# Kernel tuning notes

Measured on AMD Instinct MI355X. Metric: run time of the kernel, lower is better.

The kernel has to match this reference:

```python
import jax, jax.numpy as jnp
import numpy as np

# ---- static config (mirrors init_kwargs) ----
H, N, HKV = 32, 64, 8
HN = H * N            # model dim 2048
KV_DIM = HKV * N      # 512
B, T = 2, 1024
EPS = 1e-6
ROPE_THETA = 1.0e6
SPLITS_WAVGK = (96, 96, 64, 256, 64)   # xw, xa, xv, xg, xk lora ranks
SPLITS_RKV = (HN, KV_DIM, KV_DIM)


def rms_norm(x, w, eps=EPS):
    xf = x.astype(jnp.float32)
    var = jnp.mean(xf * xf, axis=-1, keepdims=True)
    return (w * (xf * jax.lax.rsqrt(var + eps))).astype(x.dtype)


def rotate_half(x):
    x1, x2 = jnp.split(x, 2, axis=-1)
    return jnp.concatenate((-x2, x1), axis=-1)


def apply_rope(q, k, cos, sin):
    # q:[B,T,H,N], k:[B,T,HKV,N], cos/sin:[B,T,N] -> unsqueeze head dim (unsqueeze_dim=2)
    cos = cos[:, :, None, :]
    sin = sin[:, :, None, :]
    return q * cos + rotate_half(q) * sin, k * cos + rotate_half(k) * sin


def rwkv7_recurrence(r, gk, k, v, a, b, S0):
    # fused_recurrent_rwkv7 (head_first=False). All inputs [B,T,H,N] fp32, S0 [B,H,N_key,N_val].
    # S_t = diag(exp(gk_t)) S_{t-1} + b_t (a_t^T S_{t-1}) + k_t v_t^T ;  o_t = r_t^T S_t
    def step(S, inp):
        r_t, w_t, k_t, v_t, a_t, b_t = inp
        sa = jnp.einsum('bhk,bhkv->bhv', a_t, S)
        S = (jnp.exp(w_t)[..., None] * S
             + k_t[..., None] * v_t[..., None, :]
             + b_t[..., None] * sa[..., None, :])
        o = jnp.einsum('bhk,bhkv->bhv', r_t, S)
        return S, o
    xs = tuple(jnp.swapaxes(t, 0, 1) for t in (r, gk, k, v, a, b))  # [T,B,H,N]
    S, o = jax.lax.scan(step, S0, xs)
    return jnp.swapaxes(o, 0, 1), S


def setup_inputs() -> dict:
    key = jax.random.key(0)
    ks = jax.random.split(key, 24)
    f32 = jnp.float32
    rn = lambda k, shape, s=1.0: jax.random.normal(k, shape, dtype=f32) * s

    x_in = rn(ks[0], (B, T, HN))
    v_first = rn(ks[1], (B, T, HKV, N))
    k_first = rn(ks[2], (B, T, HKV, N))
    state = jnp.zeros((B, H, N, N), f32)

    # real rope cache (faithful to get_batch_rope_cache output) at positions 0..T-1
    inv_freq = 1.0 / (ROPE_THETA ** (np.arange(0, N, 2, dtype=np.float32) / N))
    freqs = np.outer(np.arange(T, dtype=np.float32), inv_freq)  # [T, N/2]
    emb = np.concatenate([freqs, freqs], axis=-1)               # [T, N]
    calc_cos = jnp.broadcast_to(jnp.asarray(np.cos(emb), dtype=np.float32), (B, T, N))
    calc_sin = jnp.broadcast_to(jnp.asarray(np.sin(emb), dtype=np.float32), (B, T, N))

    wavgk1 = rn(ks[3], (HN, sum(SPLITS_WAVGK)), 0.02)
    w0 = rn(ks[4], (HN,), 0.5)
    w2 = rn(ks[5], (SPLITS_WAVGK[0], HN), 0.02)
    a0 = rn(ks[6], (HN,), 0.1)
    a2 = rn(ks[7], (SPLITS_WAVGK[1], HN), 0.02)
    v0 = rn(ks[8], (KV_DIM,), 0.1)
    v2 = rn(ks[9], (SPLITS_WAVGK[2], KV_DIM), 0.02)
    g2 = rn(ks[10], (SPLITS_WAVGK[3], HN), 0.02)
    k0 = rn(ks[11], (KV_DIM,), 0.1)
    k2 = rn(ks[12], (SPLITS_WAVGK[4], KV_DIM), 0.02)
    r_k = rn(ks[13], (H, N), 0.1)
    RKV = rn(ks[14], (HN, HN + 2 * KV_DIM), 0.02)   # fpx weight, dequantized form
    O = rn(ks[15], (HN, HN), 0.02)
    R_bias = rn(ks[16], (HN,), 0.02)
    K_bias = rn(ks[17], (KV_DIM,), 0.02)
    V_bias = rn(ks[18], (KV_DIM,), 0.02)
    ln_r = jnp.ones((N,), f32)
    ln_k = jnp.ones((N,), f32)
    ln1 = jnp.ones((HN,), f32)
    ln2 = jnp.ones((HN,), f32)

    return dict(x_in=x_in, v_first=v_first, k_first=k_first, state=state,
                calc_cos=calc_cos, calc_sin=calc_sin, wavgk1=wavgk1,
                w0=w0, w2=w2, a0=a0, a2=a2, v0=v0, v2=v2, g2=g2, k0=k0, k2=k2,
                r_k=r_k, RKV=RKV, O=O, R_bias=R_bias, K_bias=K_bias, V_bias=V_bias,
                ln_r=ln_r, ln_k=ln_k, ln1=ln1, ln2=ln2)


def reference(x_in, v_first, k_first, state, calc_cos, calc_sin, wavgk1,
              w0, w2, a0, a2, v0, v2, g2, k0, k2, r_k, RKV, O,
              R_bias, K_bias, V_bias, ln_r, ln_k, ln1, ln2):
    Bx, Tx, C = x_in.shape
    kv_repeat = HN // KV_DIM  # GQA repeat factor (4)

    x = rms_norm(x_in, ln1)
    xw, xa, xv, xg, xk = jnp.split(x @ wavgk1, np.cumsum(SPLITS_WAVGK)[:-1].tolist(), axis=-1)

    rkv = x @ RKV  # fpx_matmul -> dense matmul on dequantized weight
    r, k, v = jnp.split(rkv, np.cumsum(SPLITS_RKV)[:-1].tolist(), axis=-1)
    r = (r + R_bias).reshape(Bx, Tx, H, N)
    k = (k + K_bias).reshape(Bx, Tx, HKV, N)
    v = (v + V_bias).reshape(Bx, Tx, HKV, N)

    r = rms_norm(r, ln_r)
    k = rms_norm(k, ln_k)
    r, k = apply_rope(r, k, calc_cos, calc_sin)

    # layer_id = 1 (> 0): mix with first-layer value/key
    v = v + (v_first - v) * jax.nn.sigmoid(xv @ v2 + v0).reshape(Bx, Tx, HKV, N)
    k = k + (k_first - k) * jax.nn.sigmoid(xk @ k2 + k0).reshape(Bx, Tx, HKV, N)

    # repeat_kv: [B,T,HKV,N] -> [B,T,H,N] -> [B,T,HN]
    k = jnp.repeat(k, kv_repeat, axis=2).reshape(Bx, Tx, HN)
    v = jnp.repeat(v, kv_repeat, axis=2).reshape(Bx, Tx, HN)

    a = jax.nn.sigmoid(xa @ a2 + a0)  # in-context learning rate gate [B,T,HN]
    k4 = k.reshape(Bx, Tx, H, N)
    kk = (k4 / jnp.maximum(jnp.linalg.norm(k4, axis=-1, keepdims=True), 1e-12)).reshape(Bx, Tx, HN)

    w_log = -jax.nn.softplus(-(jnp.tanh(xw) @ w2 + w0)) - 0.5  # log-decay, <= -0.5
    k = k * (1.0 - w_log + a)
    aa = -kk
    bb = kk * a
    gk = -jnp.exp(w_log.astype(jnp.float32))  # passed to fused_recurrent_rwkv7 as log decay

    shp = (Bx, Tx, H, N)
    o, state_out = rwkv7_recurrence(
        r.reshape(shp).astype(jnp.float32), gk.reshape(shp),
        k.reshape(shp).astype(jnp.float32), v.reshape(shp).astype(jnp.float32),
        aa.reshape(shp).astype(jnp.float32), bb.reshape(shp).astype(jnp.float32),
        state.astype(jnp.float32))

    xx = o.reshape(Bx, Tx, HN) * (float(N) ** -0.5)
    bonus = ((r * k.reshape(shp) * r_k).sum(axis=-1, keepdims=True) * v.reshape(shp)).reshape(Bx, Tx, HN)
    xx = xx.astype(x_in.dtype) + bonus

    out = (xx * (jax.nn.sigmoid(xg) @ g2)) @ O  # fpx output projection
    x_new = x_in + out
    return rms_norm(x_new, ln2)
```

## Files before the change

### kernel.cpp

```cpp
#include <hip/hip_runtime.h>

typedef unsigned short u16;
typedef unsigned int u32;

using f32x4 = __attribute__((ext_vector_type(4))) float;
using bf16x8 = __attribute__((ext_vector_type(8))) __bf16;

#define HN 2048
#define KVD 512
#define TOKENS 2048
#define N1 3712
#define K2W 576
#define N2 7168

#define OFF_Y1   0ull
#define OFF_OO   0ull
#define OFF_XG   16777216ull
#define OFF_Y2   30408704ull
#define OFF_OUTR 30408704ull
#define OFF_BT1  89128960ull
#define OFF_XB   104333312ull
#define OFF_W2T  89128960ull
#define OFF_X2   97386496ull
#define OFF_OT   89128960ull
#define OFF_RR   112721920ull
#define OFF_DEC  129499136ull
#define OFF_KR   146276352ull
#define OFF_VV   163053568ull
#define OFF_AA   179830784ull
#define OFF_BB   196608000ull
#define OFF_PAB  213385216ull
#define OFF_PKR  230162432ull
#define WS_NEED  246939648ull

__device__ __forceinline__ u16 f2bf(float f) {
    u32 u = __float_as_uint(f);
    u32 r = u + 0x7fffu + ((u >> 16) & 1u);
    return (u16)(r >> 16);
}
__device__ __forceinline__ float sigm(float x) { return 1.f / (1.f + expf(-x)); }
__device__ __forceinline__ float wsum(float v) {
#pragma unroll
    for (int m = 32; m > 0; m >>= 1) v += __shfl_xor(v, m, 64);
    return v;
}
__device__ __forceinline__ float rowsum16(float v) {
    float t;
    t = __uint_as_float(__builtin_amdgcn_update_dpp(0, __float_as_uint(v), 0x121, 0xf, 0xf, true));
    v += t;
    t = __uint_as_float(__builtin_amdgcn_update_dpp(0, __float_as_uint(v), 0x122, 0xf, 0xf, true));
    v += t;
    t = __uint_as_float(__builtin_amdgcn_update_dpp(0, __float_as_uint(v), 0x124, 0xf, 0xf, true));
    v += t;
    t = __uint_as_float(__builtin_amdgcn_update_dpp(0, __float_as_uint(v), 0x128, 0xf, 0xf, true));
    v += t;
    return v;
}

typedef __attribute__((address_space(1))) const void glob_t;
typedef __attribute__((address_space(3))) void lds_t;
__device__ __forceinline__ void gload_lds16(const void* g, void* l) {
    __builtin_amdgcn_global_load_lds((glob_t*)g, (lds_t*)l, 16, 0, 0);
}

template<int OFF>
__device__ __forceinline__ float4 ds_read128(u32 a) {
    float4 r;
    asm volatile("ds_read_b128 %0, %1 offset:%2" : "=v"(r) : "v"(a), "i"(OFF));
    return r;
}
template<int OFF>
__device__ __forceinline__ uint4 ds_read128u(u32 a) {
    uint4 r;
    asm volatile("ds_read_b128 %0, %1 offset:%2" : "=v"(r) : "v"(a), "i"(OFF));
    return r;
}
template<int OFF>
__device__ __forceinline__ float ds_read32(u32 a) {
    float r;
    asm volatile("ds_read_b32 %0, %1 offset:%2" : "=v"(r) : "v"(a), "i"(OFF));
    return r;
}

__global__ __launch_bounds__(256) void k_prep_bt1(const float* __restrict__ wavgk1,
                                                  const float* __restrict__ RKV,
                                                  u16* __restrict__ BT1) {
    __shared__ float tile[64][65];
    const int bn = blockIdx.x >> 5;
    const int bk = blockIdx.x & 31;
    const int n0 = bn << 6, k0 = bk << 6;
    const int c = threadIdx.x & 63, q = threadIdx.x >> 6;
#pragma unroll
    for (int i = 0; i < 16; ++i) {
        const int r = (q << 4) + i;
        float v = 0.f;
        if (bn < 9)       v = wavgk1[(size_t)(k0 + r) * 576 + n0 + c];
        else if (bn < 57) v = RKV[(size_t)(k0 + r) * 3072 + (n0 + c - 576)];
        tile[r][c] = v;
    }
    __syncthreads();
#pragma unroll
    for (int i = 0; i < 16; ++i) {
        const int rw = (q << 4) + i;
        BT1[(size_t)(n0 + rw) * 2048 + k0 + c] = f2bf(tile[c][rw]);
    }
}

__global__ __launch_bounds__(256) void k_prep_w2t(const float* __restrict__ w2, const float* __restrict__ a2,
                                                  const float* __restrict__ g2, const float* __restrict__ v2,
                                                  const float* __restrict__ k2, u16* __restrict__ W2T) {
    int idx = blockIdx.x * 256 + threadIdx.x;
    int n = idx / 576, c = idx - n * 576;
    float v = 0.f;
    if (n < 2048)      { if (c < 96)              v = w2[(size_t)c * 2048 + n]; }
    else if (n < 4096) { if (c >= 96 && c < 192)  v = a2[(size_t)(c - 96) * 2048 + (n - 2048)]; }
    else if (n < 6144) { if (c >= 192 && c < 448) v = g2[(size_t)(c - 192) * 2048 + (n - 4096)]; }
    else if (n < 6656) { if (c >= 448 && c < 512) v = v2[(size_t)(c - 448) * 512 + (n - 6144)]; }
    else               { if (c >= 512)            v = k2[(size_t)(c - 512) * 512 + (n - 6656)]; }
    W2T[idx] = f2bf(v);
}

__global__ __launch_bounds__(256) void k_prep_ot(const float* __restrict__ O, u16* __restrict__ OT) {
    __shared__ float tile[64][65];
    const int bn = blockIdx.x >> 5, bk = blockIdx.x & 31;
    const int n0 = bn << 6, k0 = bk << 6;
    const int c = threadIdx.x & 63, q = threadIdx.x >> 6;
#pragma unroll
    for (int i = 0; i < 16; ++i) {
        const int r = (q << 4) + i;
        tile[r][c] = O[(size_t)(k0 + r) * 2048 + n0 + c];
    }
    __syncthreads();
#pragma unroll
    for (int i = 0; i < 16; ++i) {
        const int rw = (q << 4) + i;
        OT[(size_t)(n0 + rw) * 2048 + k0 + c] = f2bf(tile[c][rw]);
    }
}

__global__ __launch_bounds__(256) void k_rms1(const float* __restrict__ X,
                                              const float* __restrict__ ln1,
                                              u16* __restrict__ XB) {
    const int t = blockIdx.x, tid = threadIdx.x;
    const float* row = X + ((size_t)t << 11);
    float4 v0 = *(const float4*)(row + tid * 8);
    float4 v1 = *(const float4*)(row + tid * 8 + 4);
    float ss = v0.x*v0.x + v0.y*v0.y + v0.z*v0.z + v0.w*v0.w
             + v1.x*v1.x + v1.y*v1.y + v1.z*v1.z + v1.w*v1.w;
    ss = wsum(ss);
    __shared__ float red[4];
    if ((tid & 63) == 0) red[tid >> 6] = ss;
    __syncthreads();
    float scale = rsqrtf((red[0] + red[1] + red[2] + red[3]) * (1.f / 2048.f) + 1e-6f);
    float4 w0_ = *(const float4*)(ln1 + tid * 8);
    float4 w1_ = *(const float4*)(ln1 + tid * 8 + 4);
    u16* o = XB + ((size_t)t << 11) + tid * 8;
    o[0] = f2bf(v0.x * scale * w0_.x); o[1] = f2bf(v0.y * scale * w0_.y);
    o[2] = f2bf(v0.z * scale * w0_.z); o[3] = f2bf(v0.w * scale * w0_.w);
    o[4] = f2bf(v1.x * scale * w1_.x); o[5] = f2bf(v1.y * scale * w1_.y);
    o[6] = f2bf(v1.z * scale * w1_.z); o[7] = f2bf(v1.w * scale * w1_.w);
}

__global__ __launch_bounds__(256) void k_gemm(const u16* __restrict__ A,
                                              const u16* __restrict__ Bt,
                                              float* __restrict__ C,
                                              int M, int N, int K) {
    __shared__ __align__(16) u16 tA[4096];
    __shared__ __align__(16) u16 tB[4096];
    const int tid = threadIdx.x;
    const int w = tid >> 6, l = tid & 63;
    const int bm = blockIdx.x << 7, bn = blockIdx.y << 7;
    const int wm = (w >> 1) << 6, wn = (w & 1) << 6;
    const int lrow = l >> 2;
    const int lk = (((l & 3) ^ ((l >> 3) & 3)) << 3);
    f32x4 acc[4][4] = {};
    const size_t rA0 = (size_t)(bm + (w << 4) + lrow) * K;
    const size_t rA1 = (size_t)(bm + ((w + 4) << 4) + lrow) * K;
    const size_t rB0 = (size_t)(bn + (w << 4) + lrow) * K;
    const size_t rB1 = (size_t)(bn + ((w + 4) << 4) + lrow) * K;
    const int frow = l & 15;
    const int koff = (((l >> 4) ^ ((l >> 1) & 3)) << 3);
    for (int kt = 0; kt < K; kt += 32) {
        gload_lds16(A + rA0 + kt + lk, &tA[w << 9]);
        gload_lds16(A + rA1 + kt + lk, &tA[2048 + (w << 9)]);
        gload_lds16(Bt + rB0 + kt + lk, &tB[w << 9]);
        gload_lds16(Bt + rB1 + kt + lk, &tB[2048 + (w << 9)]);
        __syncthreads();
        bf16x8 av[4], bv[4];
#pragma unroll
        for (int i = 0; i < 4; ++i) {
            av[i] = *(const bf16x8*)&tA[((wm + (i << 4) + frow) << 5) + koff];
            bv[i] = *(const bf16x8*)&tB[((wn + (i << 4) + frow) << 5) + koff];
        }
#pragma unroll
        for (int i = 0; i < 4; ++i)
#pragma unroll
            for (int j = 0; j < 4; ++j)
                acc[i][j] = __builtin_amdgcn_mfma_f32_16x16x32_bf16(av[i], bv[j], acc[i][j], 0, 0, 0);
        __syncthreads();
    }
    const int crow = bm + wm + ((l >> 4) << 2);
    const int ccol = bn + wn + (l & 15);
#pragma unroll
    for (int i = 0; i < 4; ++i)
#pragma unroll
        for (int j = 0; j < 4; ++j)
#pragma unroll
            for (int jj = 0; jj < 4; ++jj)
                C[(size_t)(crow + (i << 4) + jj) * N + ccol + (j << 4)] = acc[i][j][jj];
}

__global__ __launch_bounds__(256) void k_gemm2(const u16* __restrict__ A,
                                               const u16* __restrict__ Bt,
                                               float* __restrict__ C) {
    __shared__ __align__(16) u16 tA[4096];
    __shared__ __align__(16) u16 tB[4096];
    const int tid = threadIdx.x;
    const int w = tid >> 6, l = tid & 63;
    const int by = blockIdx.y;
    int c0, K;
    if (by < 16)      { c0 = 0;   K = 96; }
    else if (by < 32) { c0 = 96;  K = 96; }
    else if (by < 48) { c0 = 192; K = 256; }
    else if (by < 52) { c0 = 448; K = 64; }
    else              { c0 = 512; K = 64; }
    const int n0 = by << 7;
    const int bm = blockIdx.x << 7;
    const int wm = (w >> 1) << 6, wn = (w & 1) << 6;
    const int lrow = l >> 2;
    const int lk = (((l & 3) ^ ((l >> 3) & 3)) << 3);
    f32x4 acc[4][4] = {};
    const size_t rA0 = (size_t)(bm + (w << 4) + lrow) * 576 + c0;
    const size_t rA1 = (size_t)(bm + ((w + 4) << 4) + lrow) * 576 + c0;
    const size_t rB0 = (size_t)(n0 + (w << 4) + lrow) * 576 + c0;
    const size_t rB1 = (size_t)(n0 + ((w + 4) << 4) + lrow) * 576 + c0;
    const int frow = l & 15;
    const int koff = (((l >> 4) ^ ((l >> 1) & 3)) << 3);
    for (int kt = 0; kt < K; kt += 32) {
        gload_lds16(A + rA0 + kt + lk, &tA[w << 9]);
        gload_lds16(A + rA1 + kt + lk, &tA[2048 + (w << 9)]);
        gload_lds16(Bt + rB0 + kt + lk, &tB[w << 9]);
        gload_lds16(Bt + rB1 + kt + lk, &tB[2048 + (w << 9)]);
        __syncthreads();
        bf16x8 av[4], bv[4];
#pragma unroll
        for (int i = 0; i < 4; ++i) {
            av[i] = *(const bf16x8*)&tA[((wm + (i << 4) + frow) << 5) + koff];
            bv[i] = *(const bf16x8*)&tB[((wn + (i << 4) + frow) << 5) + koff];
        }
#pragma unroll
        for (int i = 0; i < 4; ++i)
#pragma unroll
            for (int j = 0; j < 4; ++j)
                acc[i][j] = __builtin_amdgcn_mfma_f32_16x16x32_bf16(av[i], bv[j], acc[i][j], 0, 0, 0);
        __syncthreads();
    }
    const int crow = bm + wm + ((l >> 4) << 2);
    const int ccol = n0 + wn + (l & 15);
#pragma unroll
    for (int i = 0; i < 4; ++i)
#pragma unroll
        for (int j = 0; j < 4; ++j)
#pragma unroll
            for (int jj = 0; jj < 4; ++jj)
                C[(size_t)(crow + (i << 4) + jj) * N2 + ccol + (j << 4)] = acc[i][j][jj];
}

__global__ __launch_bounds__(256) void k_prep_x2(const float* __restrict__ Y1, u16* __restrict__ X2) {
    int idx = blockIdx.x * 256 + threadIdx.x;
    int t = idx / 576, c = idx - t * 576;
    const float* y1 = Y1 + (size_t)t * N1;
    float v;
    if (c < 96)       v = tanhf(y1[c]);
    else if (c < 192) v = y1[c];
    else if (c < 448) v = sigm(y1[c + 64]);
    else if (c < 512) v = y1[c - 256];
    else              v = y1[c];
    X2[idx] = f2bf(v);
}

__global__ __launch_bounds__(256) void k_prep_rec(
    const float* __restrict__ Y1, const float* __restrict__ Y2,
    const float* __restrict__ v_first, const float* __restrict__ k_first,
    const float* __restrict__ cosb, const float* __restrict__ sinb,
    const float* __restrict__ w0, const float* __restrict__ a0,
    const float* __restrict__ v0b, const float* __restrict__ k0b,
    const float* __restrict__ R_bias, const float* __restrict__ K_bias,
    const float* __restrict__ V_bias, const float* __restrict__ ln_r,
    const float* __restrict__ ln_k,
    float* __restrict__ RR, float* __restrict__ DEC, float* __restrict__ KR,
    float* __restrict__ VV, u32* __restrict__ PAB, u32* __restrict__ PKR) {
    const int t = blockIdx.x, tid = threadIdx.x;
    const int ww = tid >> 6, lane = tid & 63;
    const float* y1 = Y1 + (size_t)t * N1;
    const float* y2 = Y2 + (size_t)t * N2;
    const float cs = cosb[t * 64 + lane];
    const float sn = sinb[t * 64 + lane];
    const float sign = lane < 32 ? -1.f : 1.f;
    const size_t tb = (size_t)t << 11;
    __shared__ float kkv[512], vkv[512];
    float rsave[8];
#pragma unroll
    for (int i = 0; i < 8; ++i) {
        int h = ww * 8 + i, c = h * 64 + lane;
        float rr = y1[576 + c] + R_bias[c];
        float ssq = wsum(rr * rr);
        float rn = ln_r[lane] * rr * rsqrtf(ssq * (1.f / 64.f) + 1e-6f);
        float rot = sign * __shfl(rn, lane ^ 32, 64);
        rsave[i] = rn * cs + rot * sn;
        RR[tb + c] = rsave[i];
    }
#pragma unroll
    for (int i = 0; i < 2; ++i) {
        int j = ww * 2 + i, c = j * 64 + lane;
        float kr = y1[2624 + c] + K_bias[c];
        float ssq = wsum(kr * kr);
        float kn = ln_k[lane] * kr * rsqrtf(ssq * (1.f / 64.f) + 1e-6f);
        float rot = sign * __shfl(kn, lane ^ 32, 64);
        float krope = kn * cs + rot * sn;
        float ksig = sigm(y2[6656 + c] + k0b[c]);
        kkv[c] = krope + (k_first[(size_t)t * 512 + c] - krope) * ksig;
        float vr = y1[3136 + c] + V_bias[c];
        float vsig = sigm(y2[6144 + c] + v0b[c]);
        vkv[c] = vr + (v_first[(size_t)t * 512 + c] - vr) * vsig;
    }
    __syncthreads();
#pragma unroll
    for (int i = 0; i < 8; ++i) {
        int h = ww * 8 + i, c = h * 64 + lane;
        int ckv = (h >> 2) * 64 + lane;
        float kb = kkv[ckv], vb = vkv[ckv];
        float a_ = sigm(y2[2048 + c] + a0[c]);
        float wr = y2[c] + w0[c];
        float z = -wr;
        float sp = fmaxf(z, 0.f) + log1pf(expf(-fabsf(z)));
        float w_log = -sp - 0.5f;
        float ssq = wsum(kb * kb);
        float kk = kb / fmaxf(sqrtf(ssq), 1e-12f);
        const float kr2 = kb * (1.f - w_log + a_);
        DEC[tb + c] = expf(-expf(w_log));
        KR[tb + c] = kr2;
        VV[tb + c] = vb;
        PAB[tb + c] = (u32)f2bf(-kk) | ((u32)f2bf(kk * a_) << 16);
        PKR[tb + c] = (u32)f2bf(kr2) | ((u32)f2bf(rsave[i]) << 16);
    }
}

__global__ __launch_bounds__(256, 1) void k_recv14(
    const float* __restrict__ DECp, const u32* __restrict__ PABp,
    const u32* __restrict__ PKRp, const float* __restrict__ VVp,
    const float* __restrict__ S0, float* __restrict__ OO) {
    __shared__ __align__(16) float cbuf[2][4][32][64];
    const int tid = threadIdx.x;
    const int wl = tid >> 6;
    const int lane = tid & 63;
    const int vl = lane >> 4;
    const int kq = lane & 15;
    const int quarter = blockIdx.x & 3;
    const int ch = blockIdx.x >> 2;
    const int vcol = (quarter << 4) + (wl << 2) + vl;
    const size_t cb = ((size_t)(ch >> 5) * 1024 * 2048) + ((size_t)(ch & 31) << 6);

    const float* s0 = S0 + ((size_t)ch << 12);
    float L0 = s0[((kq << 2) + 0) * 64 + vcol];
    float L1 = s0[((kq << 2) + 1) * 64 + vcol];
    float L2 = s0[((kq << 2) + 2) * 64 + vcol];
    float L3 = s0[((kq << 2) + 3) * 64 + vcol];

    const int trow = (wl << 2) + vl;

#define STG(B, T0)                                                             \
    {                                                                          \
        const size_t g0 = cb + (size_t)((T0) + trow) * 2048 + (kq << 2);       \
        const size_t g1 = cb + (size_t)((T0) + 16 + trow) * 2048 + (kq << 2);  \
        float* lb = &cbuf[B][0][0][0] + (wl << 8);                             \
        gload_lds16(DECp + g0, lb);                                            \
        gload_lds16(DECp + g1, lb + 1024);                                     \
        gload_lds16(PABp + g0, lb + 2048);                                     \
        gload_lds16(PABp + g1, lb + 3072);                                     \
        gload_lds16(PKRp + g0, lb + 4096);                                     \
        gload_lds16(PKRp + g1, lb + 5120);                                     \
        gload_lds16(VVp + g0, lb + 6144);                                      \
        gload_lds16(VVp + g1, lb + 7168);                                      \
    }

    const u32 base0 = (u32)(size_t)(void*)&cbuf[0][0][0][0];
    const u32 aA0 = base0 + (kq << 4);
    const u32 aV0 = base0 + 24576 + (vcol << 2);

#define LDSTEP(J)                                                              \
    cD[J] = ds_read128<(J) * 256>(aA);                                         \
    cPA[J] = ds_read128u<8192 + (J) * 256>(aA);                                \
    cPK[J] = ds_read128u<16384 + (J) * 256>(aA);                               \
    cV[J] = ds_read32<(J) * 256>(aV);

#define UNP_LO(u) __uint_as_float((u) << 16)
#define UNP_HI(u) __uint_as_float((u) & 0xffff0000u)

    STG(0, 0);
    __syncthreads();

    for (int c = 0; c < 32; ++c) {
        const int b = c & 1;
        if (c < 31) STG(b ^ 1, (c + 1) << 5);
        u32 aA = aA0 + b * 32768;
        u32 aV = aV0 + b * 32768;
        int t = c << 5;
        for (int g = 0; g < 4; ++g) {
            float4 cD[8];
            uint4 cPA[8], cPK[8];
            float cV[8];
            LDSTEP(0) LDSTEP(1) LDSTEP(2) LDSTEP(3)
            LDSTEP(4) LDSTEP(5) LDSTEP(6) LDSTEP(7)
            asm volatile("s_waitcnt lgkmcnt(0)" ::: "memory");
            __builtin_amdgcn_sched_barrier(0);
#pragma unroll
            for (int j = 0; j < 8; ++j) {
                const float4 D4 = cD[j];
                const uint4 pa = cPA[j], pk = cPK[j];
                const float Vsj = cV[j];
                const float Ax = UNP_LO(pa.x), Ay = UNP_LO(pa.y),
                            Az = UNP_LO(pa.z), Aw = UNP_LO(pa.w);
                const float Bx = UNP_HI(pa.x), By = UNP_HI(pa.y),
                            Bz = UNP_HI(pa.z), Bw = UNP_HI(pa.w);
                const float Kx = UNP_LO(pk.x), Ky = UNP_LO(pk.y),
                            Kz = UNP_LO(pk.z), Kw = UNP_LO(pk.w);
                const float Rx = UNP_HI(pk.x), Ry = UNP_HI(pk.y),
                            Rz = UNP_HI(pk.z), Rw = UNP_HI(pk.w);
                float sp = fmaf(L1, Ay, L0 * Ax) + fmaf(L3, Aw, L2 * Az);
                const float sa = rowsum16(sp);
                L0 = fmaf(Bx, sa, fmaf(Kx, Vsj, L0 * D4.x));
                L1 = fmaf(By, sa, fmaf(Ky, Vsj, L1 * D4.y));
                L2 = fmaf(Bz, sa, fmaf(Kz, Vsj, L2 * D4.z));
                L3 = fmaf(Bw, sa, fmaf(Kw, Vsj, L3 * D4.w));
                float op = fmaf(L1, Ry, L0 * Rx) + fmaf(L3, Rw, L2 * Rz);
                const float o = rowsum16(op);
                if (kq == 0) OO[cb + ((size_t)(t + j) << 11) + vcol] = o;
            }
            t += 8;
            aA += 2048;
            aV += 2048;
        }
        __syncthreads();
    }
#undef UNP_LO
#undef UNP_HI
#undef LDSTEP
#undef STG
}

__global__ __launch_bounds__(256) void k_gate(
    const float* __restrict__ OOp, const float* __restrict__ RRp,
    const float* __restrict__ KRp, const float* __restrict__ VVp,
    const float* __restrict__ Y2, const float* __restrict__ r_k,
    u16* __restrict__ XG) {
    const int t = blockIdx.x, tid = threadIdx.x;
    const int ww = tid >> 6, lane = tid & 63;
    const size_t tb = (size_t)t << 11;
#pragma unroll
    for (int i = 0; i < 8; ++i) {
        int c = (ww * 8 + i) * 64 + lane;
        float pr = RRp[tb + c] * KRp[tb + c] * r_k[c];
        float dot = wsum(pr);
        float xx = OOp[tb + c] * 0.125f + dot * VVp[tb + c];
        float g = Y2[(size_t)t * N2 + 4096 + c];
        XG[tb + c] = f2bf(xx * g);
    }
}

__global__ __launch_bounds__(256) void k_final(const float* __restrict__ x_in,
                                               const float* __restrict__ OUTR,
                                               const float* __restrict__ ln2,
                                               float* __restrict__ out) {
    const int t = blockIdx.x, tid = threadIdx.x;
    const float* xr = x_in + ((size_t)t << 11);
    const float* orow = OUTR + ((size_t)t << 11);
    float4 a0 = *(const float4*)(xr + tid * 8);
    float4 a1 = *(const float4*)(xr + tid * 8 + 4);
    float4 b0 = *(const float4*)(orow + tid * 8);
    float4 b1 = *(const float4*)(orow + tid * 8 + 4);
    float v[8] = {a0.x + b0.x, a0.y + b0.y, a0.z + b0.z, a0.w + b0.w,
                  a1.x + b1.x, a1.y + b1.y, a1.z + b1.z, a1.w + b1.w};
    float ss = 0.f;
#pragma unroll
    for (int i = 0; i < 8; ++i) ss = fmaf(v[i], v[i], ss);
    ss = wsum(ss);
    __shared__ float red[4];
    if ((tid & 63) == 0) red[tid >> 6] = ss;
    __syncthreads();
    float scale = rsqrtf((red[0] + red[1] + red[2] + red[3]) * (1.f / 2048.f) + 1e-6f);
    float* o = out + ((size_t)t << 11) + tid * 8;
#pragma unroll
    for (int i = 0; i < 8; ++i) o[i] = ln2[tid * 8 + i] * v[i] * scale;
}

extern "C" void kernel_launch(void* const* d_in, const int* in_sizes, int n_in,
                              void* d_out, int out_size, void* d_ws, size_t ws_size,
                              hipStream_t stream) {
    const float* x_in    = (const float*)d_in[0];
    const float* v_first = (const float*)d_in[1];
    const float* k_first = (const float*)d_in[2];
    const float* state   = (const float*)d_in[3];
    const float* cosb    = (const float*)d_in[4];
    const float* sinb    = (const float*)d_in[5];
    const float* wavgk1  = (const float*)d_in[6];
    const float* w0      = (const float*)d_in[7];
    const float* w2      = (const float*)d_in[8];
    const float* a0      = (const float*)d_in[9];
    const float* a2      = (const float*)d_in[10];
    const float* v0      = (const float*)d_in[11];
    const float* v2      = (const float*)d_in[12];
    const float* g2      = (const float*)d_in[13];
    const float* k0      = (const float*)d_in[14];
    const float* k2      = (const float*)d_in[15];
    const float* r_k     = (const float*)d_in[16];
    const float* RKV     = (const float*)d_in[17];
    const float* O       = (const float*)d_in[18];
    const float* R_bias  = (const float*)d_in[19];
    const float* K_bias  = (const float*)d_in[20];
    const float* V_bias  = (const float*)d_in[21];
    const float* ln_r    = (const float*)d_in[22];
    const float* ln_k    = (const float*)d_in[23];
    const float* ln1     = (const float*)d_in[24];
    const float* ln2     = (const float*)d_in[25];

    if (ws_size < WS_NEED) return;

    char* ws = (char*)d_ws;
    u16*   BT1  = (u16*)(ws + OFF_BT1);
    u16*   W2T  = (u16*)(ws + OFF_W2T);
    u16*   OT   = (u16*)(ws + OFF_OT);
    u16*   XB   = (u16*)(ws + OFF_XB);
    float* Y1   = (float*)(ws + OFF_Y1);
    u16*   X2   = (u16*)(ws + OFF_X2);
    float* Y2   = (float*)(ws + OFF_Y2);
    float* RR   = (float*)(ws + OFF_RR);
    float* DEC  = (float*)(ws + OFF_DEC);
    float* KR   = (float*)(ws + OFF_KR);
    float* VV   = (float*)(ws + OFF_VV);
    u32*   PAB  = (u32*)(ws + OFF_PAB);
    u32*   PKR  = (u32*)(ws + OFF_PKR);
    float* OO   = (float*)(ws + OFF_OO);
    u16*   XG   = (u16*)(ws + OFF_XG);
    float* OUTR = (float*)(ws + OFF_OUTR);

    k_prep_bt1<<<1856, 256, 0, stream>>>(wavgk1, RKV, BT1);
    k_rms1<<<2048, 256, 0, stream>>>(x_in, ln1, XB);
    k_gemm<<<dim3(16, 29), 256, 0, stream>>>(XB, BT1, Y1, 2048, N1, 2048);
    k_prep_w2t<<<16128, 256, 0, stream>>>(w2, a2, g2, v2, k2, W2T);
    k_prep_x2<<<4608, 256, 0, stream>>>(Y1, X2);
    k_gemm2<<<dim3(16, 56), 256, 0, stream>>>(X2, W2T, Y2);
    k_prep_rec<<<2048, 256, 0, stream>>>(Y1, Y2, v_first, k_first, cosb, sinb,
                                         w0, a0, v0, k0, R_bias, K_bias, V_bias,
                                         ln_r, ln_k, RR, DEC, KR, VV, PAB, PKR);
    k_prep_ot<<<1024, 256, 0, stream>>>(O, OT);
    k_recv14<<<256, 256, 0, stream>>>(DEC, PAB, PKR, VV, state, OO);
    k_gate<<<2048, 256, 0, stream>>>(OO, RR, KR, VV, Y2, r_k, XG);
    k_gemm<<<dim3(16, 16), 256, 0, stream>>>(XG, OT, OUTR, 2048, 2048, 2048);
    k_final<<<2048, 256, 0, stream>>>(x_in, OUTR, ln2, (float*)d_out);
}
```

Baseline: 386.0 us.

## Software-pipeline LDS reads in recurrence and tile-transpose the W2T weight prep

```diff
diff --git a/kernel.cpp b/kernel.cpp
--- a/kernel.cpp
+++ b/kernel.cpp
@@ -109,15 +109,30 @@
 __global__ __launch_bounds__(256) void k_prep_w2t(const float* __restrict__ w2, const float* __restrict__ a2,
                                                   const float* __restrict__ g2, const float* __restrict__ v2,
                                                   const float* __restrict__ k2, u16* __restrict__ W2T) {
-    int idx = blockIdx.x * 256 + threadIdx.x;
-    int n = idx / 576, c = idx - n * 576;
-    float v = 0.f;
-    if (n < 2048)      { if (c < 96)              v = w2[(size_t)c * 2048 + n]; }
-    else if (n < 4096) { if (c >= 96 && c < 192)  v = a2[(size_t)(c - 96) * 2048 + (n - 2048)]; }
-    else if (n < 6144) { if (c >= 192 && c < 448) v = g2[(size_t)(c - 192) * 2048 + (n - 4096)]; }
-    else if (n < 6656) { if (c >= 448 && c < 512) v = v2[(size_t)(c - 448) * 512 + (n - 6144)]; }
-    else               { if (c >= 512)            v = k2[(size_t)(c - 512) * 512 + (n - 6656)]; }
-    W2T[idx] = f2bf(v);
+    __shared__ float tile[64][65];
+    const int bx = blockIdx.x;
+    const int bn = bx / 9, bc = bx - bn * 9;
+    const int n0 = bn << 6, c0 = bc << 6;
+    const int cc = threadIdx.x & 63, q = threadIdx.x >> 6;
+#pragma unroll
+    for (int i = 0; i < 16; ++i) {
+        const int r = (q << 4) + i;
+        const int c = c0 + r;
+        const int n = n0 + cc;
+        float v = 0.f;
+        if (n0 < 2048)      { if (c < 96)              v = w2[(size_t)c * 2048 + n]; }
+        else if (n0 < 4096) { if (c >= 96 && c < 192)  v = a2[(size_t)(c - 96) * 2048 + (n - 2048)]; }
+        else if (n0 < 6144) { if (c >= 192 && c < 448) v = g2[(size_t)(c - 192) * 2048 + (n - 4096)]; }
+        else if (n0 < 6656) { if (c >= 448 && c < 512) v = v2[(size_t)(c - 448) * 512 + (n - 6144)]; }
+        else                { if (c >= 512)            v = k2[(size_t)(c - 512) * 512 + (n - 6656)]; }
+        tile[r][cc] = v;
+    }
+    __syncthreads();
+#pragma unroll
+    for (int i = 0; i < 16; ++i) {
+        const int rw = (q << 4) + i;
+        W2T[(size_t)(n0 + rw) * 576 + c0 + cc] = f2bf(tile[cc][rw]);
+    }
 }
 
 __global__ __launch_bounds__(256) void k_prep_ot(const float* __restrict__ O, u16* __restrict__ OT) {
@@ -346,7 +361,7 @@
     }
 }
 
-__global__ __launch_bounds__(256, 1) void k_recv14(
+__global__ __launch_bounds__(256, 1) void k_recv16(
     const float* __restrict__ DECp, const u32* __restrict__ PABp,
     const u32* __restrict__ PKRp, const float* __restrict__ VVp,
     const float* __restrict__ S0, float* __restrict__ OO) {
@@ -388,14 +403,56 @@
     const u32 aA0 = base0 + (kq << 4);
     const u32 aV0 = base0 + 24576 + (vcol << 2);
 
-#define LDSTEP(J)                                                              \
-    cD[J] = ds_read128<(J) * 256>(aA);                                         \
-    cPA[J] = ds_read128u<8192 + (J) * 256>(aA);                                \
-    cPK[J] = ds_read128u<16384 + (J) * 256>(aA);                               \
-    cV[J] = ds_read32<(J) * 256>(aV);
+    float4 cDa0, cDa1, cDb0, cDb1;
+    uint4 cPAa0, cPAa1, cPAb0, cPAb1, cPKa0, cPKa1, cPKb0, cPKb1;
+    float cV[32];
+
+#define LD2(S_, G)                                                             \
+    cD##S_##0 = ds_read128<(G) * 512>(aAb);                                    \
+    cD##S_##1 = ds_read128<(G) * 512 + 256>(aAb);                              \
+    cPA##S_##0 = ds_read128u<8192 + (G) * 512>(aAb);                           \
+    cPA##S_##1 = ds_read128u<8192 + (G) * 512 + 256>(aAb);                     \
+    cPK##S_##0 = ds_read128u<16384 + (G) * 512>(aAb);                          \
+    cPK##S_##1 = ds_read128u<16384 + (G) * 512 + 256>(aAb);
+
+#define VRD(J) cV[J] = ds_read32<(J) * 256>(aVb);
+#define VRD8(J) VRD(J) VRD((J)+1) VRD((J)+2) VRD((J)+3) VRD((J)+4) VRD((J)+5) VRD((J)+6) VRD((J)+7)
+
+#define WAIT6 asm volatile("s_waitcnt lgkmcnt(6)" ::: "memory");               \
+    __builtin_amdgcn_sched_barrier(0);
+#define WAIT0 asm volatile("s_waitcnt lgkmcnt(0)" ::: "memory");               \
+    __builtin_amdgcn_sched_barrier(0);
 
 #define UNP_LO(u) __uint_as_float((u) << 16)
 #define UNP_HI(u) __uint_as_float((u) & 0xffff0000u)
+
+#define STEP1(D4, pa, pk, Vsj, T)                                              \
+    {                                                                          \
+        const float Ax = UNP_LO(pa.x), Ay = UNP_LO(pa.y),                      \
+                    Az = UNP_LO(pa.z), Aw = UNP_LO(pa.w);                      \
+        const float Bx = UNP_HI(pa.x), By = UNP_HI(pa.y),                      \
+                    Bz = UNP_HI(pa.z), Bw = UNP_HI(pa.w);                      \
+        const float Kx = UNP_LO(pk.x), Ky = UNP_LO(pk.y),                      \
+                    Kz = UNP_LO(pk.z), Kw = UNP_LO(pk.w);                      \
+        const float Rx = UNP_HI(pk.x), Ry = UNP_HI(pk.y),                      \
+                    Rz = UNP_HI(pk.z), Rw = UNP_HI(pk.w);                      \
+        float sp = fmaf(L1, Ay, L0 * Ax) + fmaf(L3, Aw, L2 * Az);              \
+        const float sa = rowsum16(sp);                                         \
+        L0 = fmaf(Bx, sa, fmaf(Kx, Vsj, L0 * D4.x));                           \
+        L1 = fmaf(By, sa, fmaf(Ky, Vsj, L1 * D4.y));                           \
+        L2 = fmaf(Bz, sa, fmaf(Kz, Vsj, L2 * D4.z));                           \
+        L3 = fmaf(Bw, sa, fmaf(Kw, Vsj, L3 * D4.w));                           \
+        float op = fmaf(L1, Ry, L0 * Rx) + fmaf(L3, Rw, L2 * Rz);              \
+        const float o = rowsum16(op);                                          \
+        if (kq == 0) OO[cb + ((size_t)(T) << 11) + vcol] = o;                  \
+    }
+
+#define STEP2(S_, G)                                                           \
+    STEP1(cD##S_##0, cPA##S_##0, cPK##S_##0, cV[2 * (G)], tbase + 2 * (G));    \
+    STEP1(cD##S_##1, cPA##S_##1, cPK##S_##1, cV[2 * (G) + 1], tbase + 2 * (G) + 1);
+
+#define PAIR(G)                                                                \
+    LD2(b, (G) + 1) WAIT6 STEP2(a, G) LD2(a, (G) + 2) WAIT6 STEP2(b, (G) + 1)
 
     STG(0, 0);
     __syncthreads();
@@ -403,49 +460,26 @@
     for (int c = 0; c < 32; ++c) {
         const int b = c & 1;
         if (c < 31) STG(b ^ 1, (c + 1) << 5);
-        u32 aA = aA0 + b * 32768;
-        u32 aV = aV0 + b * 32768;
-        int t = c << 5;
-        for (int g = 0; g < 4; ++g) {
-            float4 cD[8];
-            uint4 cPA[8], cPK[8];
-            float cV[8];
-            LDSTEP(0) LDSTEP(1) LDSTEP(2) LDSTEP(3)
-            LDSTEP(4) LDSTEP(5) LDSTEP(6) LDSTEP(7)
-            asm volatile("s_waitcnt lgkmcnt(0)" ::: "memory");
-            __builtin_amdgcn_sched_barrier(0);
-#pragma unroll
-            for (int j = 0; j < 8; ++j) {
-                const float4 D4 = cD[j];
-                const uint4 pa = cPA[j], pk = cPK[j];
-                const float Vsj = cV[j];
-                const float Ax = UNP_LO(pa.x), Ay = UNP_LO(pa.y),
-                            Az = UNP_LO(pa.z), Aw = UNP_LO(pa.w);
-                const float Bx = UNP_HI(pa.x), By = UNP_HI(pa.y),
-                            Bz = UNP_HI(pa.z), Bw = UNP_HI(pa.w);
-                const float Kx = UNP_LO(pk.x), Ky = UNP_LO(pk.y),
-                            Kz = UNP_LO(pk.z), Kw = UNP_LO(pk.w);
-                const float Rx = UNP_HI(pk.x), Ry = UNP_HI(pk.y),
-                            Rz = UNP_HI(pk.z), Rw = UNP_HI(pk.w);
-                float sp = fmaf(L1, Ay, L0 * Ax) + fmaf(L3, Aw, L2 * Az);
-                const float sa = rowsum16(sp);
-                L0 = fmaf(Bx, sa, fmaf(Kx, Vsj, L0 * D4.x));
-                L1 = fmaf(By, sa, fmaf(Ky, Vsj, L1 * D4.y));
-                L2 = fmaf(Bz, sa, fmaf(Kz, Vsj, L2 * D4.z));
-                L3 = fmaf(Bw, sa, fmaf(Kw, Vsj, L3 * D4.w));
-                float op = fmaf(L1, Ry, L0 * Rx) + fmaf(L3, Rw, L2 * Rz);
-                const float o = rowsum16(op);
-                if (kq == 0) OO[cb + ((size_t)(t + j) << 11) + vcol] = o;
-            }
-            t += 8;
-            aA += 2048;
-            aV += 2048;
-        }
+        const u32 aAb = aA0 + b * 32768;
+        const u32 aVb = aV0 + b * 32768;
+        const int tbase = c << 5;
+        VRD8(0) VRD8(8) VRD8(16) VRD8(24)
+        WAIT0
+        LD2(a, 0)
+        PAIR(0) PAIR(2) PAIR(4) PAIR(6) PAIR(8) PAIR(10) PAIR(12)
+        LD2(b, 15) WAIT6 STEP2(a, 14) WAIT0 STEP2(b, 15)
         __syncthreads();
     }
+#undef PAIR
+#undef STEP2
+#undef STEP1
 #undef UNP_LO
 #undef UNP_HI
-#undef LDSTEP
+#undef WAIT0
+#undef WAIT6
+#undef VRD8
+#undef VRD
+#undef LD2
 #undef STG
 }
 
@@ -547,14 +581,14 @@
     k_prep_bt1<<<1856, 256, 0, stream>>>(wavgk1, RKV, BT1);
     k_rms1<<<2048, 256, 0, stream>>>(x_in, ln1, XB);
     k_gemm<<<dim3(16, 29), 256, 0, stream>>>(XB, BT1, Y1, 2048, N1, 2048);
-    k_prep_w2t<<<16128, 256, 0, stream>>>(w2, a2, g2, v2, k2, W2T);
+    k_prep_w2t<<<1008, 256, 0, stream>>>(w2, a2, g2, v2, k2, W2T);
     k_prep_x2<<<4608, 256, 0, stream>>>(Y1, X2);
     k_gemm2<<<dim3(16, 56), 256, 0, stream>>>(X2, W2T, Y2);
     k_prep_rec<<<2048, 256, 0, stream>>>(Y1, Y2, v_first, k_first, cosb, sinb,
                                          w0, a0, v0, k0, R_bias, K_bias, V_bias,
                                          ln_r, ln_k, RR, DEC, KR, VV, PAB, PKR);
     k_prep_ot<<<1024, 256, 0, stream>>>(O, OT);
-    k_recv14<<<256, 256, 0, stream>>>(DEC, PAB, PKR, VV, state, OO);
+    k_recv16<<<256, 256, 0, stream>>>(DEC, PAB, PKR, VV, state, OO);
     k_gate<<<2048, 256, 0, stream>>>(OO, RR, KR, VV, Y2, r_k, XG);
     k_gemm<<<dim3(16, 16), 256, 0, stream>>>(XG, OT, OUTR, 2048, 2048, 2048);
     k_final<<<2048, 256, 0, stream>>>(x_in, OUTR, ln2, (float*)d_out);
```

After: 376.9 us. 1.02x faster.
